# Optimization experiments

Measured on AMD Instinct MI355X. Metric: run time of the kernel, lower is better.

## Reference

```python
import jax, jax.numpy as jnp
import numpy as np

B, C, H, W = 8, 256, 64, 64
CI = C // 2  # inter_channels


def setup_inputs() -> dict:
    key = jax.random.key(0)
    ks = jax.random.split(key, 9)
    s_in = 1.0 / np.sqrt(C)
    s_ci = 1.0 / np.sqrt(CI)
    return {
        "x": jax.random.normal(ks[0], (B, C, H, W), dtype=jnp.float32),
        "g_w": jax.random.uniform(ks[1], (CI, C), jnp.float32, -s_in, s_in),
        "g_b": jax.random.uniform(ks[2], (CI,), jnp.float32, -s_in, s_in),
        "theta_w": jax.random.uniform(ks[3], (CI, C), jnp.float32, -s_in, s_in),
        "theta_b": jax.random.uniform(ks[4], (CI,), jnp.float32, -s_in, s_in),
        "phi_w": jax.random.uniform(ks[5], (CI, C), jnp.float32, -s_in, s_in),
        "phi_b": jax.random.uniform(ks[6], (CI,), jnp.float32, -s_in, s_in),
        "W_w": jax.random.uniform(ks[7], (C, CI), jnp.float32, -s_ci, s_ci),
        "W_b": jax.random.uniform(ks[8], (C,), jnp.float32, -s_ci, s_ci),
    }


def reference(x, g_w, g_b, theta_w, theta_b, phi_w, phi_b, W_w, W_b):
    b, c, h, w = x.shape
    xf = x.reshape(b, c, h * w)  # [B, C, N]
    # 1x1 convs == per-pixel linear maps
    g_x = jnp.einsum("oc,bcn->bon", g_w, xf) + g_b[:, None]      # [B, CI, N]
    theta_x = jnp.einsum("oc,bcn->bon", theta_w, xf) + theta_b[:, None]
    phi_x = jnp.einsum("oc,bcn->bon", phi_w, xf) + phi_b[:, None]
    # attention_map[b, i, j] = <theta[:, i], phi[:, j]>, softmax over j
    attn = jax.nn.softmax(jnp.einsum("bci,bcj->bij", theta_x, phi_x), axis=-1)
    # y[b, c, i] = sum_j g_x[b, c, j] * attn[b, i, j]
    y = jnp.einsum("bcj,bij->bci", g_x, attn)  # [B, CI, N]
    out = jnp.einsum("oc,bcn->bon", W_w, y) + W_b[:, None]  # [B, C, N]
    return out.reshape(b, c, h, w) + x
```

## Files before the change

### kernel.cpp

```cpp
#include <hip/hip_runtime.h>
#include <hip/hip_bf16.h>

#define B_  8
#define C_  256
#define CI_ 128
#define N_  4096

typedef __bf16 bf16;
typedef __attribute__((ext_vector_type(8))) __bf16 bf16x8;
typedef __attribute__((ext_vector_type(4))) __bf16 bf16x4;
typedef __attribute__((ext_vector_type(4))) float  floatx4;

static_assert(sizeof(bf16) == 2, "bf16 size");

__device__ inline floatx4 mfma16(bf16x8 a, bf16x8 b, floatx4 c) {
    return __builtin_amdgcn_mfma_f32_16x16x32_bf16(a, b, c, 0, 0, 0);
}

__device__ inline bool detect_fp32(const void* probe) {
    const unsigned short* u = (const unsigned short*)probe;
    int lane = threadIdx.x & 63;
    unsigned short w = u[lane * 2];
    int ex = (w >> 7) & 0xFF;
    bool insane = !((ex > 96 && ex < 143) || (w & 0x7FFF) == 0);
    unsigned long long b = __ballot(insane);
    return __popcll(b) > 16;
}

__device__ inline bf16x8 load8(const void* p, size_t i, bool fp32) {
    if (!fp32) return *(const bf16x8*)((const bf16*)p + i);
    const float* f = (const float*)p + i;
    floatx4 a = *(const floatx4*)(f);
    floatx4 c = *(const floatx4*)(f + 4);
    bf16x8 r;
    r[0] = (bf16)a[0]; r[1] = (bf16)a[1]; r[2] = (bf16)a[2]; r[3] = (bf16)a[3];
    r[4] = (bf16)c[0]; r[5] = (bf16)c[1]; r[6] = (bf16)c[2]; r[7] = (bf16)c[3];
    return r;
}

__device__ inline float loadv(const void* p, size_t i, bool fp32) {
    return fp32 ? ((const float*)p)[i] : (float)((const bf16*)p)[i];
}

__device__ inline bf16x8 cvt8(floatx4 a, floatx4 b) {
    bf16x8 r;
    r[0] = (bf16)a[0]; r[1] = (bf16)a[1]; r[2] = (bf16)a[2]; r[3] = (bf16)a[3];
    r[4] = (bf16)b[0]; r[5] = (bf16)b[1]; r[6] = (bf16)b[2]; r[7] = (bf16)b[3];
    return r;
}

__global__ __launch_bounds__(512) void proj3_kernel(
    const void* __restrict__ x,
    const void* __restrict__ wt, const void* __restrict__ bt,
    const void* __restrict__ wp, const void* __restrict__ bp,
    const void* __restrict__ wg, const void* __restrict__ bg,
    bf16* __restrict__ T, bf16* __restrict__ P, bf16* __restrict__ G)
{
    const bool fp32 = detect_fp32(x);

    const int b  = blockIdx.y;
    const int n0 = blockIdx.x * 128;

    __shared__ bf16 xT[128][40];
    __shared__ bf16 wl[384][40];

    const int t    = threadIdx.x;
    const int w    = t >> 6;
    const int lane = t & 63;
    const int l15  = lane & 15;
    const int quad = lane >> 4;
    const int wm   = w >> 1;
    const int wn   = w & 1;

    const int sc = t >> 4;
    const int sm = t & 15;
    const int wr = t >> 2;
    const int wc = (t & 3) * 8;

    floatx4 acc[6][4];
#pragma unroll
    for (int f = 0; f < 6; ++f)
#pragma unroll
        for (int ni = 0; ni < 4; ++ni) acc[f][ni] = (floatx4)0.f;

    floatx4 pxa, pxb; bf16x8 pxh;
    floatx4 pwa[3], pwb[3]; bf16x8 pwh[3];

    auto issue = [&](int k) {
        size_t xo = ((size_t)b * C_ + k + sc) * N_ + n0 + sm * 8;
        if (fp32) {
            const float* fx_ = (const float*)x + xo;
            pxa = *(const floatx4*)fx_;
            pxb = *(const floatx4*)(fx_ + 4);
        } else {
            pxh = *(const bf16x8*)((const bf16*)x + xo);
        }
#pragma unroll
        for (int p = 0; p < 3; ++p) {
            const void* ws = (p == 0) ? wt : (p == 1) ? wp : wg;
            size_t wo = (size_t)wr * C_ + k + wc;
            if (fp32) {
                const float* fw_ = (const float*)ws + wo;
                pwa[p] = *(const floatx4*)fw_;
                pwb[p] = *(const floatx4*)(fw_ + 4);
            } else {
                pwh[p] = *(const bf16x8*)((const bf16*)ws + wo);
            }
        }
    };

    issue(0);

    for (int ks = 0; ks < 8; ++ks) {
        {
            bf16x8 xv = fp32 ? cvt8(pxa, pxb) : pxh;
            int colx = ((((sc >> 3) + sm) & 3) << 3) + (sc & 7);
#pragma unroll
            for (int i = 0; i < 8; ++i) xT[sm * 8 + i][colx] = xv[i];
#pragma unroll
            for (int p = 0; p < 3; ++p) {
                bf16x8 wv = fp32 ? cvt8(pwa[p], pwb[p]) : pwh[p];
                *(bf16x8*)(&wl[p * 128 + wr][wc]) = wv;
            }
        }
        __syncthreads();

        if (ks < 7) issue((ks + 1) * 32);

        bf16x8 fxr[4], fwr[6];
#pragma unroll
        for (int ni = 0; ni < 4; ++ni) {
            int px = wn * 64 + ni * 16 + l15;
            int ch = (quad + (px >> 3)) & 3;
            fxr[ni] = *(const bf16x8*)(&xT[px][ch * 8]);
        }
#pragma unroll
        for (int f = 0; f < 6; ++f)
            fwr[f] = *(const bf16x8*)(&wl[f * 64 + wm * 16 + l15][quad * 8]);

#pragma unroll
        for (int f = 0; f < 4; ++f)
#pragma unroll
            for (int ni = 0; ni < 4; ++ni)
                acc[f][ni] = mfma16(fxr[ni], fwr[f], acc[f][ni]);
#pragma unroll
        for (int f = 4; f < 6; ++f)
#pragma unroll
            for (int ni = 0; ni < 4; ++ni)
                acc[f][ni] = mfma16(fwr[f], fxr[ni], acc[f][ni]);

        __syncthreads();
    }

#pragma unroll
    for (int f = 0; f < 6; ++f) {
        const void* bsel = (f < 2) ? bt : (f < 4) ? bp : bg;
        if (f < 4) {
            bf16* outp = ((f < 2) ? T : P) + (size_t)b * N_ * CI_;
            int o = (f & 1) * 64 + wm * 16 + l15;
            float bv = loadv(bsel, o, fp32);
#pragma unroll
            for (int ni = 0; ni < 4; ++ni)
#pragma unroll
                for (int r = 0; r < 4; ++r) {
                    int px = n0 + wn * 64 + ni * 16 + quad * 4 + r;
                    outp[(size_t)px * CI_ + o] = (bf16)(acc[f][ni][r] + bv);
                }
        } else {
            bf16* outp = G + (size_t)b * CI_ * N_;
#pragma unroll
            for (int r = 0; r < 4; ++r) {
                int o = (f & 1) * 64 + wm * 16 + quad * 4 + r;
                float bv = loadv(bsel, o, fp32);
#pragma unroll
                for (int ni = 0; ni < 4; ++ni) {
                    int px = n0 + wn * 64 + ni * 16 + l15;
                    outp[(size_t)o * N_ + px] = (bf16)(acc[f][ni][r] + bv);
                }
            }
        }
    }
}

__global__ __launch_bounds__(512) void attn_kernel(
    const bf16* __restrict__ T,
    const bf16* __restrict__ P,
    const bf16* __restrict__ G,
    const void* __restrict__ Ww,
    const void* __restrict__ Wb,
    const void* __restrict__ x,
    void* __restrict__ out)
{
    const int bid = blockIdx.x;
    const int b   = bid & 7;
    const int i0  = (bid >> 3) * 128;

    __shared__ __align__(16) char smem[143360];

    const bool fp32 = detect_fp32(x);

    const int t    = threadIdx.x;
    const int w    = t >> 6;
    const int g    = w >> 2;
    const int wg   = w & 3;
    const int tg   = t & 255;
    const int lane = t & 63;
    const int l15  = lane & 15;
    const int quad = lane >> 4;

    bf16* Kl = (bf16*)(smem + g * 35840);
    bf16* Vt = (bf16*)(smem + g * 35840 + 17408);
    bf16* Pw = (bf16*)(smem + 71680 + w * 4608);

    const bf16* Kb = P + (size_t)b * N_ * CI_;
    const bf16* Vb = G + (size_t)b * CI_ * N_;
    const int jbase = g * 2048;

    bf16x8 qf[2][4];
#pragma unroll
    for (int rf = 0; rf < 2; ++rf) {
        const bf16* Qb = T + ((size_t)b * N_ + i0 + wg * 32 + rf * 16 + l15) * CI_;
#pragma unroll
        for (int ks = 0; ks < 4; ++ks)
            qf[rf][ks] = *(const bf16x8*)(Qb + ks * 32 + quad * 8);
    }

    floatx4 O[2][8];
#pragma unroll
    for (int rf = 0; rf < 2; ++rf)
#pragma unroll
        for (int cf = 0; cf < 8; ++cf) O[rf][cf] = (floatx4)0.f;
    float lsum[2][4];
#pragma unroll
    for (int rf = 0; rf < 2; ++rf)
#pragma unroll
        for (int r = 0; r < 4; ++r) lsum[rf][r] = 0.f;

    bf16x8 kreg[4], vreg[4];
#pragma unroll
    for (int s = 0; s < 4; ++s) {
        int id = tg + s * 256;
        kreg[s] = *(const bf16x8*)(Kb + (size_t)(jbase + (id >> 4)) * CI_ + (id & 15) * 8);
        vreg[s] = *(const bf16x8*)(Vb + (size_t)(id >> 3) * N_ + jbase + (id & 7) * 8);
    }

    for (int it = 0; it < 32; ++it) {
#pragma unroll
        for (int s = 0; s < 4; ++s) {
            int id = tg + s * 256;
            *(bf16x8*)(Kl + (id >> 4) * 136 + (id & 15) * 8) = kreg[s];
            *(bf16x8*)(Vt + (id >> 3) * 72 + (id & 7) * 8) = vreg[s];
        }
        __syncthreads();

        if (it < 31) {
            int j0n = jbase + (it + 1) * 64;
#pragma unroll
            for (int s = 0; s < 4; ++s) {
                int id = tg + s * 256;
                kreg[s] = *(const bf16x8*)(Kb + (size_t)(j0n + (id >> 4)) * CI_ + (id & 15) * 8);
                vreg[s] = *(const bf16x8*)(Vb + (size_t)(id >> 3) * N_ + j0n + (id & 7) * 8);
            }
        }

        floatx4 S[2][4];
#pragma unroll
        for (int jf = 0; jf < 4; ++jf) {
            floatx4 s0 = (floatx4)0.f, s1 = (floatx4)0.f;
#pragma unroll
            for (int ks = 0; ks < 4; ++ks) {
                bf16x8 kf = *(const bf16x8*)(Kl + (jf * 16 + l15) * 136 + ks * 32 + quad * 8);
                s0 = mfma16(qf[0][ks], kf, s0);
                s1 = mfma16(qf[1][ks], kf, s1);
            }
            S[0][jf] = s0;
            S[1][jf] = s1;
        }

#pragma unroll
        for (int rf = 0; rf < 2; ++rf)
#pragma unroll
            for (int r = 0; r < 4; ++r) {
                float p0 = __expf(S[rf][0][r]);
                float p1 = __expf(S[rf][1][r]);
                float p2 = __expf(S[rf][2][r]);
                float p3 = __expf(S[rf][3][r]);
                lsum[rf][r] += (p0 + p1) + (p2 + p3);
                int row = rf * 16 + quad * 4 + r;
                Pw[row * 72 + 0 * 16 + l15] = (bf16)p0;
                Pw[row * 72 + 1 * 16 + l15] = (bf16)p1;
                Pw[row * 72 + 2 * 16 + l15] = (bf16)p2;
                Pw[row * 72 + 3 * 16 + l15] = (bf16)p3;
            }

#pragma unroll
        for (int ks = 0; ks < 2; ++ks) {
            bf16x8 pf0 = *(const bf16x8*)(Pw + l15 * 72 + ks * 32 + quad * 8);
            bf16x8 pf1 = *(const bf16x8*)(Pw + (16 + l15) * 72 + ks * 32 + quad * 8);
#pragma unroll
            for (int cf = 0; cf < 8; ++cf) {
                bf16x8 vf = *(const bf16x8*)(Vt + (cf * 16 + l15) * 72 + ks * 32 + quad * 8);
                O[0][cf] = mfma16(pf0, vf, O[0][cf]);
                O[1][cf] = mfma16(pf1, vf, O[1][cf]);
            }
        }
        __syncthreads();
    }

    float* scrO = (float*)smem;
    float* scrL = (float*)(smem + 71680);
    bf16*  Yl   = (bf16*)(smem + 108544);
    if (g == 1) {
#pragma unroll
        for (int rf = 0; rf < 2; ++rf)
#pragma unroll
            for (int cf = 0; cf < 8; ++cf)
#pragma unroll
                for (int r = 0; r < 4; ++r)
                    scrO[(rf * 32 + cf * 4 + r) * 256 + wg * 64 + lane] = O[rf][cf][r];
#pragma unroll
        for (int rf = 0; rf < 2; ++rf)
#pragma unroll
            for (int r = 0; r < 4; ++r)
                scrL[(rf * 4 + r) * 256 + wg * 64 + lane] = lsum[rf][r];
    }
    __syncthreads();
    if (g == 0) {
#pragma unroll
        for (int rf = 0; rf < 2; ++rf)
#pragma unroll
            for (int cf = 0; cf < 8; ++cf)
#pragma unroll
                for (int r = 0; r < 4; ++r)
                    O[rf][cf][r] += scrO[(rf * 32 + cf * 4 + r) * 256 + wg * 64 + lane];

#pragma unroll
        for (int rf = 0; rf < 2; ++rf)
#pragma unroll
            for (int r = 0; r < 4; ++r) {
                float rs = lsum[rf][r] + scrL[(rf * 4 + r) * 256 + wg * 64 + lane];
                rs += __shfl_xor(rs, 1);
                rs += __shfl_xor(rs, 2);
                rs += __shfl_xor(rs, 4);
                rs += __shfl_xor(rs, 8);
                lsum[rf][r] = 1.f / rs;
            }

#pragma unroll
        for (int rf = 0; rf < 2; ++rf)
#pragma unroll
            for (int cf = 0; cf < 8; ++cf)
#pragma unroll
                for (int r = 0; r < 4; ++r) {
                    int px = wg * 32 + rf * 16 + quad * 4 + r;
                    Yl[px * 136 + cf * 16 + l15] =
                        (bf16)(O[rf][cf][r] * lsum[rf][r]);
                }
    }
    __syncthreads();

    bf16* Wl = (bf16*)smem;
#pragma unroll
    for (int p = 0; p < 16; ++p) {
        int idx = p * 2048 + t * 4;
        int o   = idx >> 7;
        int ci  = idx & 127;
        bf16x4 v;
        if (fp32) {
            floatx4 f4 = *(const floatx4*)((const float*)Ww + idx);
            v[0] = (bf16)f4[0]; v[1] = (bf16)f4[1];
            v[2] = (bf16)f4[2]; v[3] = (bf16)f4[3];
        } else {
            v = *(const bf16x4*)((const bf16*)Ww + idx);
        }
        *(bf16x4*)(&Wl[o * 136 + ci]) = v;
    }
    __syncthreads();

    {
        const int wm = w >> 1;
        const int wn = w & 1;
        floatx4 acc[4][4];
#pragma unroll
        for (int i = 0; i < 4; ++i)
#pragma unroll
            for (int j = 0; j < 4; ++j) acc[i][j] = (floatx4)0.f;

#pragma unroll
        for (int ks = 0; ks < 4; ++ks) {
            bf16x8 fa[4], fb[4];
#pragma unroll
            for (int i = 0; i < 4; ++i) {
                fa[i] = *(const bf16x8*)(&Wl[(wm * 64 + i * 16 + l15) * 136 + ks * 32 + quad * 8]);
                fb[i] = *(const bf16x8*)(&Yl[(wn * 64 + i * 16 + l15) * 136 + ks * 32 + quad * 8]);
            }
#pragma unroll
            for (int mi = 0; mi < 4; ++mi)
#pragma unroll
                for (int ni = 0; ni < 4; ++ni)
                    acc[mi][ni] = mfma16(fa[mi], fb[ni], acc[mi][ni]);
        }

#pragma unroll
        for (int mi = 0; mi < 4; ++mi)
#pragma unroll
            for (int ni = 0; ni < 4; ++ni)
#pragma unroll
                for (int r = 0; r < 4; ++r) {
                    int oo = wm * 64 + mi * 16 + quad * 4 + r;
                    int px = i0 + wn * 64 + ni * 16 + l15;
                    size_t idx = ((size_t)b * C_ + oo) * N_ + px;
                    float v = acc[mi][ni][r] + loadv(Wb, oo, fp32)
                            + loadv(x, idx, fp32);
                    if (fp32) ((float*)out)[idx] = v;
                    else      ((bf16*)out)[idx] = (bf16)v;
                }
    }
}

extern "C" void kernel_launch(void* const* d_in, const int* in_sizes, int n_in,
                              void* d_out, int out_size, void* d_ws, size_t ws_size,
                              hipStream_t stream) {
    const void* x    = d_in[0];
    const void* g_w  = d_in[1];
    const void* g_b  = d_in[2];
    const void* th_w = d_in[3];
    const void* th_b = d_in[4];
    const void* ph_w = d_in[5];
    const void* ph_b = d_in[6];
    const void* W_w  = d_in[7];
    const void* W_b  = d_in[8];

    const size_t plane = (size_t)B_ * N_ * CI_;
    bf16* T = (bf16*)d_ws;
    bf16* P = T + plane;
    bf16* G = P + plane;

    proj3_kernel<<<dim3(N_ / 128, B_), 512, 0, stream>>>(
        x, th_w, th_b, ph_w, ph_b, g_w, g_b, T, P, G);
    attn_kernel<<<dim3(N_ / 128 * B_), 512, 0, stream>>>(
        T, P, G, W_w, W_b, x, d_out);
}
```

Before: 214.6 us.

## Load projection weights straight into MFMA registers and halve the pixel tile

The projection kernel now works on 64-pixel tiles with 256 threads and asks for 2 blocks per CU. Each wave loads its weight fragments directly from global memory into registers in MFMA operand layout, so the shared-memory weight staging buffer and its stores and loads go away. This shrinks LDS use and doubles the grid size, which may improve occupancy. In exchange, weights are re-read from global memory or cache by more blocks, and each wave holds more prefetch registers.

New measurement: 223.9 us. 1.04x slower.

```diff
diff --git a/kernel.cpp b/kernel.cpp
--- a/kernel.cpp
+++ b/kernel.cpp
@@ -49,7 +49,7 @@
     return r;
 }
 
-__global__ __launch_bounds__(512) void proj3_kernel(
+__global__ __launch_bounds__(256, 2) void proj4_kernel(
     const void* __restrict__ x,
     const void* __restrict__ wt, const void* __restrict__ bt,
     const void* __restrict__ wp, const void* __restrict__ bp,
@@ -59,23 +59,18 @@
     const bool fp32 = detect_fp32(x);
 
     const int b  = blockIdx.y;
-    const int n0 = blockIdx.x * 128;
-
-    __shared__ bf16 xT[128][40];
-    __shared__ bf16 wl[384][40];
+    const int n0 = blockIdx.x * 64;
+
+    __shared__ bf16 xT[64][40];
 
     const int t    = threadIdx.x;
     const int w    = t >> 6;
     const int lane = t & 63;
     const int l15  = lane & 15;
     const int quad = lane >> 4;
-    const int wm   = w >> 1;
-    const int wn   = w & 1;
-
-    const int sc = t >> 4;
-    const int sm = t & 15;
-    const int wr = t >> 2;
-    const int wc = (t & 3) * 8;
+
+    const int ch  = t >> 3;
+    const int oct = t & 7;
 
     floatx4 acc[6][4];
 #pragma unroll
@@ -83,60 +78,64 @@
 #pragma unroll
         for (int ni = 0; ni < 4; ++ni) acc[f][ni] = (floatx4)0.f;
 
-    floatx4 pxa, pxb; bf16x8 pxh;
-    floatx4 pwa[3], pwb[3]; bf16x8 pwh[3];
-
-    auto issue = [&](int k) {
-        size_t xo = ((size_t)b * C_ + k + sc) * N_ + n0 + sm * 8;
+    floatx4 xpa, xpb; bf16x8 xph;
+    floatx4 wpa[6], wpb[6]; bf16x8 wph[6];
+
+    auto issue_x = [&](int k) {
+        size_t xo = ((size_t)b * C_ + k + ch) * N_ + n0 + oct * 8;
         if (fp32) {
             const float* fx_ = (const float*)x + xo;
-            pxa = *(const floatx4*)fx_;
-            pxb = *(const floatx4*)(fx_ + 4);
+            xpa = *(const floatx4*)fx_;
+            xpb = *(const floatx4*)(fx_ + 4);
         } else {
-            pxh = *(const bf16x8*)((const bf16*)x + xo);
-        }
-#pragma unroll
-        for (int p = 0; p < 3; ++p) {
-            const void* ws = (p == 0) ? wt : (p == 1) ? wp : wg;
-            size_t wo = (size_t)wr * C_ + k + wc;
+            xph = *(const bf16x8*)((const bf16*)x + xo);
+        }
+    };
+    auto issue_w = [&](int k) {
+#pragma unroll
+        for (int f = 0; f < 6; ++f) {
+            const void* ws = (f < 2) ? wt : (f < 4) ? wp : wg;
+            int orow  = (f & 1) * 64 + w * 16 + l15;
+            size_t wo = (size_t)orow * C_ + k + quad * 8;
             if (fp32) {
                 const float* fw_ = (const float*)ws + wo;
-                pwa[p] = *(const floatx4*)fw_;
-                pwb[p] = *(const floatx4*)(fw_ + 4);
+                wpa[f] = *(const floatx4*)fw_;
+                wpb[f] = *(const floatx4*)(fw_ + 4);
             } else {
-                pwh[p] = *(const bf16x8*)((const bf16*)ws + wo);
+                wph[f] = *(const bf16x8*)((const bf16*)ws + wo);
             }
         }
     };
 
-    issue(0);
+    issue_x(0);
+    issue_w(0);
 
     for (int ks = 0; ks < 8; ++ks) {
         {
-            bf16x8 xv = fp32 ? cvt8(pxa, pxb) : pxh;
-            int colx = ((((sc >> 3) + sm) & 3) << 3) + (sc & 7);
-#pragma unroll
-            for (int i = 0; i < 8; ++i) xT[sm * 8 + i][colx] = xv[i];
-#pragma unroll
-            for (int p = 0; p < 3; ++p) {
-                bf16x8 wv = fp32 ? cvt8(pwa[p], pwb[p]) : pwh[p];
-                *(bf16x8*)(&wl[p * 128 + wr][wc]) = wv;
-            }
+            bf16x8 xv = fp32 ? cvt8(xpa, xpb) : xph;
+            int colx = ((((ch >> 3) + oct) & 3) << 3) + (ch & 7);
+#pragma unroll
+            for (int i = 0; i < 8; ++i) xT[oct * 8 + i][colx] = xv[i];
         }
         __syncthreads();
 
-        if (ks < 7) issue((ks + 1) * 32);
-
-        bf16x8 fxr[4], fwr[6];
+        bf16x8 fwr[6];
+#pragma unroll
+        for (int f = 0; f < 6; ++f)
+            fwr[f] = fp32 ? cvt8(wpa[f], wpb[f]) : wph[f];
+
+        if (ks < 7) {
+            issue_x((ks + 1) * 32);
+            issue_w((ks + 1) * 32);
+        }
+
+        bf16x8 fxr[4];
 #pragma unroll
         for (int ni = 0; ni < 4; ++ni) {
-            int px = wn * 64 + ni * 16 + l15;
-            int ch = (quad + (px >> 3)) & 3;
-            fxr[ni] = *(const bf16x8*)(&xT[px][ch * 8]);
-        }
-#pragma unroll
-        for (int f = 0; f < 6; ++f)
-            fwr[f] = *(const bf16x8*)(&wl[f * 64 + wm * 16 + l15][quad * 8]);
+            int px = ni * 16 + l15;
+            int cc = (quad + (px >> 3)) & 3;
+            fxr[ni] = *(const bf16x8*)(&xT[px][cc * 8]);
+        }
 
 #pragma unroll
         for (int f = 0; f < 4; ++f)
@@ -157,24 +156,24 @@
         const void* bsel = (f < 2) ? bt : (f < 4) ? bp : bg;
         if (f < 4) {
             bf16* outp = ((f < 2) ? T : P) + (size_t)b * N_ * CI_;
-            int o = (f & 1) * 64 + wm * 16 + l15;
+            int o = (f & 1) * 64 + w * 16 + l15;
             float bv = loadv(bsel, o, fp32);
 #pragma unroll
             for (int ni = 0; ni < 4; ++ni)
 #pragma unroll
                 for (int r = 0; r < 4; ++r) {
-                    int px = n0 + wn * 64 + ni * 16 + quad * 4 + r;
+                    int px = n0 + ni * 16 + quad * 4 + r;
                     outp[(size_t)px * CI_ + o] = (bf16)(acc[f][ni][r] + bv);
                 }
         } else {
             bf16* outp = G + (size_t)b * CI_ * N_;
 #pragma unroll
             for (int r = 0; r < 4; ++r) {
-                int o = (f & 1) * 64 + wm * 16 + quad * 4 + r;
+                int o = (f & 1) * 64 + w * 16 + quad * 4 + r;
                 float bv = loadv(bsel, o, fp32);
 #pragma unroll
                 for (int ni = 0; ni < 4; ++ni) {
-                    int px = n0 + wn * 64 + ni * 16 + l15;
+                    int px = n0 + ni * 16 + l15;
                     outp[(size_t)o * N_ + px] = (bf16)(acc[f][ni][r] + bv);
                 }
             }
@@ -436,7 +435,7 @@
     bf16* P = T + plane;
     bf16* G = P + plane;
 
-    proj3_kernel<<<dim3(N_ / 128, B_), 512, 0, stream>>>(
+    proj4_kernel<<<dim3(N_ / 64, B_), 256, 0, stream>>>(
         x, th_w, th_b, ph_w, ph_b, g_w, g_b, T, P, G);
     attn_kernel<<<dim3(N_ / 128 * B_), 512, 0, stream>>>(
         T, P, G, W_w, W_b, x, d_out);
```

## Fuse projection and attention kernels with a device-wide atomic grid barrier

Applied to the files above, without the earlier changes.

Merges the projection kernel into the attention kernel. Each block computes theta, phi and g for its own 128 pixels, keeps theta in LDS as the query tile, and writes phi and g to global memory through coalesced LDS-staged stores. A global atomic counter then acts as a grid barrier before the attention phase. This removes a kernel launch and the global round trip for T, but adds a memset launch. It relies on all 256 blocks being co-resident, which risks deadlock if occupancy does not allow that.

Result: slower. 279.8 us (+30.4%).

```diff
diff --git a/kernel.cpp b/kernel.cpp
--- a/kernel.cpp
+++ b/kernel.cpp
@@ -49,181 +49,196 @@
     return r;
 }
 
-__global__ __launch_bounds__(512) void proj3_kernel(
+__global__ __launch_bounds__(512) void fused_kernel(
     const void* __restrict__ x,
-    const void* __restrict__ wt, const void* __restrict__ bt,
-    const void* __restrict__ wp, const void* __restrict__ bp,
-    const void* __restrict__ wg, const void* __restrict__ bg,
-    bf16* __restrict__ T, bf16* __restrict__ P, bf16* __restrict__ G)
+    const void* __restrict__ th_w, const void* __restrict__ th_b,
+    const void* __restrict__ ph_w, const void* __restrict__ ph_b,
+    const void* __restrict__ g_w,  const void* __restrict__ g_b,
+    const void* __restrict__ Ww,   const void* __restrict__ Wb,
+    bf16* __restrict__ Pg,
+    bf16* __restrict__ Gg,
+    unsigned* __restrict__ cnt,
+    void* __restrict__ out)
 {
+    const int bid = blockIdx.x;
+    const int b   = bid & 7;
+    const int i0  = (bid >> 3) * 128;
+
+    __shared__ __align__(16) char smem[143360];
+
     const bool fp32 = detect_fp32(x);
-
-    const int b  = blockIdx.y;
-    const int n0 = blockIdx.x * 128;
-
-    __shared__ bf16 xT[128][40];
-    __shared__ bf16 wl[384][40];
 
     const int t    = threadIdx.x;
     const int w    = t >> 6;
     const int lane = t & 63;
     const int l15  = lane & 15;
     const int quad = lane >> 4;
-    const int wm   = w >> 1;
-    const int wn   = w & 1;
-
-    const int sc = t >> 4;
-    const int sm = t & 15;
-    const int wr = t >> 2;
-    const int wc = (t & 3) * 8;
-
-    floatx4 acc[6][4];
-#pragma unroll
-    for (int f = 0; f < 6; ++f)
-#pragma unroll
-        for (int ni = 0; ni < 4; ++ni) acc[f][ni] = (floatx4)0.f;
-
-    floatx4 pxa, pxb; bf16x8 pxh;
-    floatx4 pwa[3], pwb[3]; bf16x8 pwh[3];
-
-    auto issue = [&](int k) {
-        size_t xo = ((size_t)b * C_ + k + sc) * N_ + n0 + sm * 8;
-        if (fp32) {
-            const float* fx_ = (const float*)x + xo;
-            pxa = *(const floatx4*)fx_;
-            pxb = *(const floatx4*)(fx_ + 4);
-        } else {
-            pxh = *(const bf16x8*)((const bf16*)x + xo);
-        }
-#pragma unroll
-        for (int p = 0; p < 3; ++p) {
-            const void* ws = (p == 0) ? wt : (p == 1) ? wp : wg;
-            size_t wo = (size_t)wr * C_ + k + wc;
+
+    bf16* Tl = (bf16*)(smem + 108544);
+
+    {
+        bf16* xT = (bf16*)(smem);
+        bf16* wl = (bf16*)(smem + 10240);
+        bf16* Pl = (bf16*)(smem + 40960);
+        bf16* Gl = (bf16*)(smem + 73728);
+
+        const int wm = w >> 1;
+        const int wn = w & 1;
+        const int sc = t >> 4;
+        const int sm = t & 15;
+        const int wr = t >> 2;
+        const int wc = (t & 3) * 8;
+
+        floatx4 acc[6][4];
+#pragma unroll
+        for (int f = 0; f < 6; ++f)
+#pragma unroll
+            for (int ni = 0; ni < 4; ++ni) acc[f][ni] = (floatx4)0.f;
+
+        floatx4 pxa, pxb; bf16x8 pxh;
+        floatx4 pwa[3], pwb[3]; bf16x8 pwh[3];
+
+        auto issue = [&](int k) {
+            size_t xo = ((size_t)b * C_ + k + sc) * N_ + i0 + sm * 8;
             if (fp32) {
-                const float* fw_ = (const float*)ws + wo;
-                pwa[p] = *(const floatx4*)fw_;
-                pwb[p] = *(const floatx4*)(fw_ + 4);
+                const float* fx_ = (const float*)x + xo;
+                pxa = *(const floatx4*)fx_;
+                pxb = *(const floatx4*)(fx_ + 4);
             } else {
-                pwh[p] = *(const bf16x8*)((const bf16*)ws + wo);
-            }
-        }
-    };
-
-    issue(0);
-
-    for (int ks = 0; ks < 8; ++ks) {
+                pxh = *(const bf16x8*)((const bf16*)x + xo);
+            }
+#pragma unroll
+            for (int p = 0; p < 3; ++p) {
+                const void* ws = (p == 0) ? th_w : (p == 1) ? ph_w : g_w;
+                size_t wo = (size_t)wr * C_ + k + wc;
+                if (fp32) {
+                    const float* fw_ = (const float*)ws + wo;
+                    pwa[p] = *(const floatx4*)fw_;
+                    pwb[p] = *(const floatx4*)(fw_ + 4);
+                } else {
+                    pwh[p] = *(const bf16x8*)((const bf16*)ws + wo);
+                }
+            }
+        };
+
+        issue(0);
+
+        for (int ks = 0; ks < 8; ++ks) {
+            {
+                bf16x8 xv = fp32 ? cvt8(pxa, pxb) : pxh;
+                int colx = ((((sc >> 3) + sm) & 3) << 3) + (sc & 7);
+#pragma unroll
+                for (int i = 0; i < 8; ++i) xT[(sm * 8 + i) * 40 + colx] = xv[i];
+#pragma unroll
+                for (int p = 0; p < 3; ++p) {
+                    bf16x8 wv = fp32 ? cvt8(pwa[p], pwb[p]) : pwh[p];
+                    *(bf16x8*)(&wl[(p * 128 + wr) * 40 + wc]) = wv;
+                }
+            }
+            __syncthreads();
+
+            if (ks < 7) issue((ks + 1) * 32);
+
+            bf16x8 fxr[4], fwr[6];
+#pragma unroll
+            for (int ni = 0; ni < 4; ++ni) {
+                int px = wn * 64 + ni * 16 + l15;
+                int ch = (quad + (px >> 3)) & 3;
+                fxr[ni] = *(const bf16x8*)(&xT[px * 40 + ch * 8]);
+            }
+#pragma unroll
+            for (int f = 0; f < 6; ++f)
+                fwr[f] = *(const bf16x8*)(&wl[(f * 64 + wm * 16 + l15) * 40 + quad * 8]);
+
+#pragma unroll
+            for (int f = 0; f < 4; ++f)
+#pragma unroll
+                for (int ni = 0; ni < 4; ++ni)
+                    acc[f][ni] = mfma16(fxr[ni], fwr[f], acc[f][ni]);
+#pragma unroll
+            for (int f = 4; f < 6; ++f)
+#pragma unroll
+                for (int ni = 0; ni < 4; ++ni)
+                    acc[f][ni] = mfma16(fwr[f], fxr[ni], acc[f][ni]);
+
+            __syncthreads();
+        }
+
+#pragma unroll
+        for (int f = 0; f < 6; ++f) {
+            if (f < 4) {
+                int o = (f & 1) * 64 + wm * 16 + l15;
+                float bv = loadv((f < 2) ? th_b : ph_b, o, fp32);
+                bf16* dst   = (f < 2) ? Tl : Pl;
+                int   strd  = (f < 2) ? 136 : 128;
+#pragma unroll
+                for (int ni = 0; ni < 4; ++ni)
+#pragma unroll
+                    for (int r = 0; r < 4; ++r) {
+                        int pxl = wn * 64 + ni * 16 + quad * 4 + r;
+                        dst[pxl * strd + o] = (bf16)(acc[f][ni][r] + bv);
+                    }
+            } else {
+#pragma unroll
+                for (int r = 0; r < 4; ++r) {
+                    int o = (f & 1) * 64 + wm * 16 + quad * 4 + r;
+                    float bv = loadv(g_b, o, fp32);
+#pragma unroll
+                    for (int ni = 0; ni < 4; ++ni) {
+                        int pxl = wn * 64 + ni * 16 + l15;
+                        Gl[o * 128 + pxl] = (bf16)(acc[f][ni][r] + bv);
+                    }
+                }
+            }
+        }
+        __syncthreads();
+
         {
-            bf16x8 xv = fp32 ? cvt8(pxa, pxb) : pxh;
-            int colx = ((((sc >> 3) + sm) & 3) << 3) + (sc & 7);
-#pragma unroll
-            for (int i = 0; i < 8; ++i) xT[sm * 8 + i][colx] = xv[i];
-#pragma unroll
-            for (int p = 0; p < 3; ++p) {
-                bf16x8 wv = fp32 ? cvt8(pwa[p], pwb[p]) : pwh[p];
-                *(bf16x8*)(&wl[p * 128 + wr][wc]) = wv;
-            }
-        }
-        __syncthreads();
-
-        if (ks < 7) issue((ks + 1) * 32);
-
-        bf16x8 fxr[4], fwr[6];
-#pragma unroll
-        for (int ni = 0; ni < 4; ++ni) {
-            int px = wn * 64 + ni * 16 + l15;
-            int ch = (quad + (px >> 3)) & 3;
-            fxr[ni] = *(const bf16x8*)(&xT[px][ch * 8]);
-        }
-#pragma unroll
-        for (int f = 0; f < 6; ++f)
-            fwr[f] = *(const bf16x8*)(&wl[f * 64 + wm * 16 + l15][quad * 8]);
-
-#pragma unroll
-        for (int f = 0; f < 4; ++f)
-#pragma unroll
-            for (int ni = 0; ni < 4; ++ni)
-                acc[f][ni] = mfma16(fxr[ni], fwr[f], acc[f][ni]);
-#pragma unroll
-        for (int f = 4; f < 6; ++f)
-#pragma unroll
-            for (int ni = 0; ni < 4; ++ni)
-                acc[f][ni] = mfma16(fwr[f], fxr[ni], acc[f][ni]);
-
-        __syncthreads();
-    }
-
-#pragma unroll
-    for (int f = 0; f < 6; ++f) {
-        const void* bsel = (f < 2) ? bt : (f < 4) ? bp : bg;
-        if (f < 4) {
-            bf16* outp = ((f < 2) ? T : P) + (size_t)b * N_ * CI_;
-            int o = (f & 1) * 64 + wm * 16 + l15;
-            float bv = loadv(bsel, o, fp32);
-#pragma unroll
-            for (int ni = 0; ni < 4; ++ni)
-#pragma unroll
-                for (int r = 0; r < 4; ++r) {
-                    int px = n0 + wn * 64 + ni * 16 + quad * 4 + r;
-                    outp[(size_t)px * CI_ + o] = (bf16)(acc[f][ni][r] + bv);
-                }
-        } else {
-            bf16* outp = G + (size_t)b * CI_ * N_;
-#pragma unroll
-            for (int r = 0; r < 4; ++r) {
-                int o = (f & 1) * 64 + wm * 16 + quad * 4 + r;
-                float bv = loadv(bsel, o, fp32);
-#pragma unroll
-                for (int ni = 0; ni < 4; ++ni) {
-                    int px = n0 + wn * 64 + ni * 16 + l15;
-                    outp[(size_t)o * N_ + px] = (bf16)(acc[f][ni][r] + bv);
-                }
-            }
-        }
-    }
-}
-
-__global__ __launch_bounds__(512) void attn_kernel(
-    const bf16* __restrict__ T,
-    const bf16* __restrict__ P,
-    const bf16* __restrict__ G,
-    const void* __restrict__ Ww,
-    const void* __restrict__ Wb,
-    const void* __restrict__ x,
-    void* __restrict__ out)
-{
-    const int bid = blockIdx.x;
-    const int b   = bid & 7;
-    const int i0  = (bid >> 3) * 128;
-
-    __shared__ __align__(16) char smem[143360];
-
-    const bool fp32 = detect_fp32(x);
-
-    const int t    = threadIdx.x;
-    const int w    = t >> 6;
-    const int g    = w >> 2;
-    const int wg   = w & 3;
-    const int tg   = t & 255;
-    const int lane = t & 63;
-    const int l15  = lane & 15;
-    const int quad = lane >> 4;
+            char* Pls  = smem + 40960;
+            char* Gls  = smem + 73728;
+            char* Pdst = (char*)(Pg + ((size_t)b * N_ + i0) * CI_);
+            char* Gdst = (char*)(Gg + (size_t)b * CI_ * N_ + i0);
+#pragma unroll
+            for (int j = 0; j < 4; ++j) {
+                int off = j * 8192 + t * 16;
+                *(bf16x8*)(Pdst + off) = *(const bf16x8*)(Pls + off);
+                int o  = off >> 8;
+                int wi = off & 255;
+                *(bf16x8*)(Gdst + (size_t)o * (N_ * 2) + wi) =
+                    *(const bf16x8*)(Gls + off);
+            }
+        }
+    }
+
+    const int g  = w >> 2;
+    const int wg = w & 3;
+    const int tg = t & 255;
+
+    bf16x8 qf[2][4];
+#pragma unroll
+    for (int rf = 0; rf < 2; ++rf) {
+        int row = wg * 32 + rf * 16 + l15;
+#pragma unroll
+        for (int ks = 0; ks < 4; ++ks)
+            qf[rf][ks] = *(const bf16x8*)(&Tl[row * 136 + ks * 32 + quad * 8]);
+    }
+
+    __threadfence();
+    __syncthreads();
+    if (t == 0) {
+        __hip_atomic_fetch_add(cnt, 1u, __ATOMIC_ACQ_REL, __HIP_MEMORY_SCOPE_AGENT);
+        while (__hip_atomic_load(cnt, __ATOMIC_ACQUIRE, __HIP_MEMORY_SCOPE_AGENT) < 256u)
+            __builtin_amdgcn_s_sleep(8);
+    }
+    __syncthreads();
 
     bf16* Kl = (bf16*)(smem + g * 35840);
     bf16* Vt = (bf16*)(smem + g * 35840 + 17408);
     bf16* Pw = (bf16*)(smem + 71680 + w * 4608);
 
-    const bf16* Kb = P + (size_t)b * N_ * CI_;
-    const bf16* Vb = G + (size_t)b * CI_ * N_;
+    const bf16* Kb = Pg + (size_t)b * N_ * CI_;
+    const bf16* Vb = Gg + (size_t)b * CI_ * N_;
     const int jbase = g * 2048;
-
-    bf16x8 qf[2][4];
-#pragma unroll
-    for (int rf = 0; rf < 2; ++rf) {
-        const bf16* Qb = T + ((size_t)b * N_ + i0 + wg * 32 + rf * 16 + l15) * CI_;
-#pragma unroll
-        for (int ks = 0; ks < 4; ++ks)
-            qf[rf][ks] = *(const bf16x8*)(Qb + ks * 32 + quad * 8);
-    }
 
     floatx4 O[2][8];
 #pragma unroll
@@ -432,12 +447,11 @@
     const void* W_b  = d_in[8];
 
     const size_t plane = (size_t)B_ * N_ * CI_;
-    bf16* T = (bf16*)d_ws;
-    bf16* P = T + plane;
-    bf16* G = P + plane;
-
-    proj3_kernel<<<dim3(N_ / 128, B_), 512, 0, stream>>>(
-        x, th_w, th_b, ph_w, ph_b, g_w, g_b, T, P, G);
-    attn_kernel<<<dim3(N_ / 128 * B_), 512, 0, stream>>>(
-        T, P, G, W_w, W_b, x, d_out);
-}
+    bf16* Pg = (bf16*)d_ws;
+    bf16* Gg = Pg + plane;
+    unsigned* cnt = (unsigned*)(Gg + plane);
+
+    hipMemsetAsync(cnt, 0, sizeof(unsigned), stream);
+    fused_kernel<<<dim3(N_ / 128 * B_), 512, 0, stream>>>(
+        x, th_w, th_b, ph_w, ph_b, g_w, g_b, W_w, W_b, Pg, Gg, cnt, d_out);
+}
```
